# Kernel optimization log

Hardware: AMD Instinct MI355X
Metric: run time of the kernel (lower is better)

Reference implementation:

```python
import jax, jax.numpy as jnp
import numpy as np

H = 256
EPS = 1e-5
RBF_GAMMA = 10.0
RBF_CENTERS = jnp.asarray(np.arange(0.0, np.pi, 0.1), dtype=jnp.float32)  # 32 centers


def layer_norm(x, g, b):
    m = x.mean(-1, keepdims=True)
    v = ((x - m) ** 2).mean(-1, keepdims=True)
    return (x - m) * jax.lax.rsqrt(v + EPS) * g + b


def gin(src, dst, n_nodes, node_feat, edge_feat, w1, b1, w2, b2):
    # message = h_src + h_edge ; sum-aggregate at dst ; 2-layer MLP
    msg = node_feat[src] + edge_feat                                  # [E, H]
    agg = jax.ops.segment_sum(msg, dst, num_segments=n_nodes)        # [N, H]
    return jax.nn.relu(agg @ w1 + b1) @ w2 + b2


def graph_normal(gid, n_graphs, x):
    # divide each node feature by sqrt(#nodes in its graph)
    cnt = jax.ops.segment_sum(jnp.ones((x.shape[0],), x.dtype), gid, num_segments=n_graphs)
    return x * jax.lax.rsqrt(jnp.maximum(cnt, 1.0))[gid][:, None]


def geognn_block(src, dst, gid, n_graphs, node_hidden, edge_feat, w1, b1, w2, b2, ln_g, ln_b):
    out = gin(src, dst, node_hidden.shape[0], node_hidden, edge_feat, w1, b1, w2, b2)
    out = layer_norm(out, ln_g, ln_b)
    out = graph_normal(gid, n_graphs, out)
    # activation=False, dropout is identity in eval mode
    return out + node_hidden


def setup_inputs() -> dict:
    key = jax.random.key(0)
    ks = jax.random.split(key, 24)
    N, E, A, G = 65536, 131072, 262144, 2048
    nC = RBF_CENTERS.shape[0]
    s = 1.0 / np.sqrt(H)
    inp = {
        "node_hidden": jax.random.normal(ks[0], (N, H), jnp.float32),
        "edge_hidden": jax.random.normal(ks[1], (E, H), jnp.float32),
        "bond_angle": jax.random.uniform(ks[2], (A,), jnp.float32) * np.float32(np.pi),
        "ab_src": jax.random.randint(ks[3], (N * 2,), 0, N).astype(jnp.int64)[:E],
        "ab_dst": jax.random.randint(ks[4], (E,), 0, N).astype(jnp.int64),
        "ba_src": jax.random.randint(ks[5], (A,), 0, E).astype(jnp.int64),
        "ba_dst": jax.random.randint(ks[6], (A,), 0, E).astype(jnp.int64),
        "node_gid": jnp.sort(jax.random.randint(ks[7], (N,), 0, G)).astype(jnp.int64),
        "bond_gid": jnp.sort(jax.random.randint(ks[8], (E,), 0, G)).astype(jnp.int64),
        "num_graphs": G,
        # bond-angle RBF linear
        "rbf_w": jax.random.normal(ks[9], (nC, H), jnp.float32) / np.sqrt(nC),
        "rbf_b": jnp.zeros((H,), jnp.float32),
        # bond_angle_gnn (GIN MLP + LayerNorm)
        "ba_w1": jax.random.normal(ks[10], (H, 2 * H), jnp.float32) * s,
        "ba_b1": jnp.zeros((2 * H,), jnp.float32),
        "ba_w2": jax.random.normal(ks[11], (2 * H, H), jnp.float32) * s,
        "ba_b2": jnp.zeros((H,), jnp.float32),
        "ba_ln_g": jnp.ones((H,), jnp.float32),
        "ba_ln_b": jnp.zeros((H,), jnp.float32),
        # atom_bond_gnn
        "ab_w1": jax.random.normal(ks[12], (H, 2 * H), jnp.float32) * s,
        "ab_b1": jnp.zeros((2 * H,), jnp.float32),
        "ab_w2": jax.random.normal(ks[13], (2 * H, H), jnp.float32) * s,
        "ab_b2": jnp.zeros((H,), jnp.float32),
        "ab_ln_g": jnp.ones((H,), jnp.float32),
        "ab_ln_b": jnp.zeros((H,), jnp.float32),
    }
    return inp


def reference(node_hidden, edge_hidden, bond_angle, ab_src, ab_dst, ba_src, ba_dst,
              node_gid, bond_gid, num_graphs, rbf_w, rbf_b,
              ba_w1, ba_b1, ba_w2, ba_b2, ba_ln_g, ba_ln_b,
              ab_w1, ab_b1, ab_w2, ab_b2, ab_ln_g, ab_ln_b):
    # RBF encode bond angles -> angle edge features [A, H]
    rbf = jnp.exp(-RBF_GAMMA * (bond_angle[:, None] - RBF_CENTERS[None, :]) ** 2)
    angle_hidden = rbf @ rbf_w + rbf_b
    # bond-angle GNN updates bond features (nodes of bond_angle graph)
    edge_out = geognn_block(ba_src, ba_dst, bond_gid, num_graphs,
                            edge_hidden, angle_hidden,
                            ba_w1, ba_b1, ba_w2, ba_b2, ba_ln_g, ba_ln_b)
    # atom-bond GNN updates atom features using updated bond features as edge feats
    node_out = geognn_block(ab_src, ab_dst, node_gid, num_graphs,
                            node_hidden, edge_out,
                            ab_w1, ab_b1, ab_w2, ab_b2, ab_ln_g, ab_ln_b)
    # average pooling over atoms per graph
    cnt = jax.ops.segment_sum(jnp.ones((node_out.shape[0],), node_out.dtype), node_gid,
                              num_segments=num_graphs)
    graph_repr = jax.ops.segment_sum(node_out, node_gid, num_segments=num_graphs) / jnp.maximum(cnt, 1.0)[:, None]
    return node_out, edge_out, graph_repr
```

## Files before the change

kernel.cpp:

```cpp
#include <hip/hip_runtime.h>

#define HDIM 256
#define LNEPS 1e-5f

typedef float f32x4 __attribute__((ext_vector_type(4)));
typedef short bf16x8 __attribute__((ext_vector_type(8)));

static __device__ __forceinline__ unsigned short f2b(float f) {
  union { float f; unsigned u; } v; v.f = f;
  return (unsigned short)((v.u + 0x7fffu + ((v.u >> 16) & 1u)) >> 16);
}
static __device__ __forceinline__ unsigned pk2(float lo, float hi) {
  return (unsigned)f2b(lo) | ((unsigned)f2b(hi) << 16);
}

__global__ void pack_all_kernel(const float* __restrict__ w1a, const float* __restrict__ w2a,
                                const float* __restrict__ w1b, const float* __restrict__ w2b,
                                unsigned short* __restrict__ o1a, unsigned short* __restrict__ o2a,
                                unsigned short* __restrict__ o1b, unsigned short* __restrict__ o2b) {
  int sel = blockIdx.x >> 9;
  int o = (blockIdx.x & 511) * 256 + threadIdx.x;
  int ke = o & 7, lane = (o >> 3) & 63, tt = (o >> 9) & 1, w = (o >> 10) & 3, sl = o >> 12;
  int l15 = lane & 15, lg = lane >> 4;
  if (sel == 0 || sel == 2) {
    const float* in = (sel == 0) ? w1a : w1b;
    unsigned short* out = (sel == 0) ? o1a : o1b;
    int h = sl >> 3, kk = sl & 7;
    int n1 = h * 128 + w * 32 + tt * 16 + l15;
    int k = kk * 32 + lg * 8 + ke;
    out[o] = f2b(in[k * 512 + n1]);
  } else {
    const float* in = (sel == 1) ? w2a : w2b;
    unsigned short* out = (sel == 1) ? o2a : o2b;
    int h = sl >> 3, q = sl & 7, h2 = q >> 2, kk2 = q & 3;
    int n2 = h2 * 128 + w * 32 + tt * 16 + l15;
    int k2 = h * 128 + kk2 * 32 + lg * 8 + ke;
    out[o] = f2b(in[k2 * 256 + n2]);
  }
}

__global__ void prep_kernel(const int* __restrict__ node_gid, const int* __restrict__ bond_gid,
                            const int* __restrict__ ab_dst, const int* __restrict__ ba_dst,
                            int* cnt_node, int* cnt_bond, int* deg_n, int* deg_e,
                            int N, int E, int A) {
  int i = blockIdx.x * 256 + threadIdx.x;
  if (i < N) atomicAdd(&cnt_node[node_gid[i]], 1);
  if (i < E) {
    atomicAdd(&cnt_bond[bond_gid[i]], 1);
    atomicAdd(&deg_n[ab_dst[i]], 1);
  }
  if (i < A) atomicAdd(&deg_e[ba_dst[i]], 1);
}

__global__ void scan1_both_kernel(const int* __restrict__ degE, const int* __restrict__ degN,
                                  int* __restrict__ offE, int* __restrict__ offN,
                                  int* __restrict__ bsum, int E, int N, int nbE) {
  int b = blockIdx.x;
  const int* deg; int* excl; int* bs; int n; int bb;
  if (b < nbE) { deg = degE; excl = offE; bs = bsum; n = E; bb = b; }
  else { deg = degN; excl = offN; bs = bsum + 512; n = N; bb = b - nbE; }
  int t = threadIdx.x;
  int i = bb * 256 + t;
  int v = (i < n) ? deg[i] : 0;
  int lane = t & 63, w = t >> 6;
  int s = v;
#pragma unroll
  for (int d = 1; d < 64; d <<= 1) {
    int u = __shfl_up(s, d);
    if (lane >= d) s += u;
  }
  __shared__ int wsum[4];
  if (lane == 63) wsum[w] = s;
  __syncthreads();
  int base = 0;
  for (int ww = 0; ww < w; ++ww) base += wsum[ww];
  if (i < n) excl[i] = base + s - v;
  if (t == 255) bs[bb] = base + s;
}

__global__ void scan2_both_kernel(int* __restrict__ bsum, int nbE, int nbN) {
  int* bs = bsum + blockIdx.x * 512;
  int nb = (blockIdx.x == 0) ? nbE : nbN;
  int t = threadIdx.x;
  int v = (t < nb) ? bs[t] : 0;
  int lane = t & 63, w = t >> 6;
  int s = v;
#pragma unroll
  for (int d = 1; d < 64; d <<= 1) {
    int u = __shfl_up(s, d);
    if (lane >= d) s += u;
  }
  __shared__ int wsum[16];
  if (lane == 63) wsum[w] = s;
  __syncthreads();
  int base = 0;
  for (int ww = 0; ww < w; ++ww) base += wsum[ww];
  if (t < nb) bs[t] = base + s - v;
}

__global__ void scan3f_kernel(int* __restrict__ offE, int* __restrict__ offN,
                              const int* __restrict__ bsum,
                              const int* __restrict__ cnt_node, const int* __restrict__ cnt_bond,
                              float* fac_node, float* fac_bond, float* recip_node,
                              int E, int N, int G, int nbE, int nbN) {
  int b = blockIdx.x;
  if (b < nbE) {
    int i = b * 256 + threadIdx.x;
    if (i < E) offE[i] += bsum[b];
  } else if (b < nbE + nbN) {
    int bb = b - nbE;
    int i = bb * 256 + threadIdx.x;
    if (i < N) offN[i] += bsum[512 + bb];
  } else {
    int g = (b - nbE - nbN) * 256 + threadIdx.x;
    if (g < G) {
      float cn = fmaxf((float)cnt_node[g], 1.f);
      float cb = fmaxf((float)cnt_bond[g], 1.f);
      fac_node[g] = rsqrtf(cn);
      fac_bond[g] = rsqrtf(cb);
      recip_node[g] = 1.f / cn;
    }
  }
}

__global__ void fill_both_kernel(const int* __restrict__ ba_dst, const int* __restrict__ ab_dst,
                                 const int* __restrict__ offE, const int* __restrict__ offN,
                                 int* __restrict__ curE, int* __restrict__ curN,
                                 int* __restrict__ csrE, int* __restrict__ csrN,
                                 int A, int E, int nbA) {
  int b = blockIdx.x;
  if (b < nbA) {
    int i = b * 256 + threadIdx.x;
    if (i < A) {
      int d = ba_dst[i];
      int p = atomicAdd(&curE[d], 1);
      csrE[offE[d] + p] = i;
    }
  } else {
    int i = (b - nbA) * 256 + threadIdx.x;
    if (i < E) {
      int d = ab_dst[i];
      int p = atomicAdd(&curN[d], 1);
      csrN[offN[d] + p] = i;
    }
  }
}

__global__ __launch_bounds__(256) void angle_gather_kernel(
    const float* __restrict__ bond_angle, const int* __restrict__ ba_src,
    const float* __restrict__ edge_hidden,
    const int* __restrict__ off, const int* __restrict__ deg, const int* __restrict__ csr,
    const float* __restrict__ rbf_w, const float* __restrict__ rbf_b,
    float* __restrict__ agg_e, int E) {
  __shared__ float rbfw_s[32 * 256];
  int t = threadIdx.x;
  int w = t >> 6, lane = t & 63;
#pragma unroll
  for (int i = 0; i < 8; ++i)
    *(f32x4*)&rbfw_s[(t + i * 256) * 4] = *(const f32x4*)&rbf_w[(t + i * 256) * 4];
  __syncthreads();
  int c4 = lane * 4;
  f32x4 bv = *(const f32x4*)&rbf_b[c4];
  float cc = 0.1f * (float)(lane & 31);
  for (int rr = 0; rr < 4; ++rr) {
    int d = blockIdx.x * 16 + w * 4 + rr;
    if (d >= E) break;
    int start = off[d], cnt = deg[d];
    f32x4 acc = (f32x4)0.f;
    float rbfs = 0.f;
    for (int base = 0; base < cnt; base += 64) {
      int n = cnt - base; if (n > 64) n = 64;
      float av = 0.f;
      int s = 0;
      if (lane < n) {
        int a = csr[start + base + lane];
        av = bond_angle[a];
        s = ba_src[a];
      }
#pragma unroll 4
      for (int i = 0; i < n; ++i) {
        float avi = __shfl(av, i);
        int si = __shfl(s, i);
        if (lane < 32) {
          float dd = avi - cc;
          rbfs += __expf(-10.f * dd * dd);
        }
        acc += *(const f32x4*)&edge_hidden[(size_t)si * HDIM + c4];
      }
    }
#pragma unroll 8
    for (int k = 0; k < 32; ++k) {
      float rv = __shfl(rbfs, k);
      f32x4 wv = *(const f32x4*)&rbfw_s[k * 256 + c4];
      acc[0] += rv * wv[0]; acc[1] += rv * wv[1];
      acc[2] += rv * wv[2]; acc[3] += rv * wv[3];
    }
    float fc = (float)cnt;
    acc[0] += fc * bv[0]; acc[1] += fc * bv[1];
    acc[2] += fc * bv[2]; acc[3] += fc * bv[3];
    *(f32x4*)&agg_e[(size_t)d * HDIM + c4] = acc;
  }
}

__global__ __launch_bounds__(256) void node_gather_kernel(
    const float* __restrict__ node_hidden, const float* __restrict__ edge_out,
    const int* __restrict__ ab_src,
    const int* __restrict__ off, const int* __restrict__ deg, const int* __restrict__ csr,
    float* __restrict__ agg_n, int N) {
  int w = threadIdx.x >> 6, lane = threadIdx.x & 63;
  int d = blockIdx.x * 4 + w;
  if (d >= N) return;
  int c4 = lane * 4;
  int start = off[d], cnt = deg[d];
  f32x4 acc = (f32x4)0.f;
  for (int base = 0; base < cnt; base += 64) {
    int n = cnt - base; if (n > 64) n = 64;
    int e = 0, s = 0;
    if (lane < n) {
      e = csr[start + base + lane];
      s = ab_src[e];
    }
#pragma unroll 4
    for (int i = 0; i < n; ++i) {
      int ei = __shfl(e, i);
      int si = __shfl(s, i);
      f32x4 a = *(const f32x4*)&edge_out[(size_t)ei * HDIM + c4];
      f32x4 b = *(const f32x4*)&node_hidden[(size_t)si * HDIM + c4];
      acc += a;
      acc += b;
    }
  }
  *(f32x4*)&agg_n[(size_t)d * HDIM + c4] = acc;
}

template <int POOL>
__global__ __launch_bounds__(256, 4) void mlp_kernel(
    const float* agg_in, float* out_rows,
    const float* __restrict__ residual, const int* __restrict__ gid,
    const float* __restrict__ gfactor, const float* __restrict__ grecip,
    const unsigned short* __restrict__ w1p, const float* __restrict__ b1,
    const unsigned short* __restrict__ w2p, const float* __restrict__ b2,
    const float* __restrict__ ln_g, const float* __restrict__ ln_b,
    float* pool_out, int M) {
  __shared__ __align__(16) char smem[34432];
  char* Xb = smem;
  char* Hb = smem + 16384;
  char* OutsB = smem;
  float* psA = (float*)(smem + 32768);
  float* psB = (float*)(smem + 33280);
  float* fstat = (float*)(smem + 33792);
  float* gfs = (float*)(smem + 34048);
  float* grs = (float*)(smem + 34176);
  int* gid_s = (int*)(smem + 34304);

  int t = threadIdx.x;
  int row0 = blockIdx.x * 32;
  int w = t >> 6, lane = t & 63;
  int l15 = lane & 15, lg = lane >> 4;

  const unsigned short* w1f = w1p + ((size_t)(w * 2) * 64 + lane) * 8;
  const unsigned short* w2f = w2p + ((size_t)(w * 2) * 64 + lane) * 8;
#define W1F(hh, kk, tt) (*(const bf16x8*)(w1f + (size_t)((hh) * 8 + (kk)) * 4096 + (tt) * 512))
#define W2F(hh, q, nf) (*(const bf16x8*)(w2f + (size_t)((hh) * 8 + (q)) * 4096 + (nf) * 512))

  bf16x8 wcur0, wcur1, wnxt0, wnxt1;
  wcur0 = W1F(0, 0, 0);
  wcur1 = W1F(0, 0, 1);

  {
    int row = t >> 3;
    int c0 = (t & 7) * 32;
    int gr = row0 + row; if (gr >= M) gr = M - 1;
    const float* src = agg_in + (size_t)gr * HDIM + c0;
#pragma unroll
    for (int i = 0; i < 4; ++i) {
      f32x4 a = *(const f32x4*)(src + i * 8);
      f32x4 b = *(const f32x4*)(src + i * 8 + 4);
      int byte = (row * 512 + (c0 + i * 8) * 2) ^ ((row & 7) << 4);
      *(uint4*)(Xb + byte) =
          make_uint4(pk2(a[0], a[1]), pk2(a[2], a[3]), pk2(b[0], b[1]), pk2(b[2], b[3]));
    }
  }
  __syncthreads();

  f32x4 acc2[2][4];
#pragma unroll
  for (int mt = 0; mt < 2; ++mt)
#pragma unroll
    for (int nf = 0; nf < 4; ++nf) acc2[mt][nf] = (f32x4)0.f;

  for (int h = 0; h < 4; ++h) {
    f32x4 acc1[2][2];
#pragma unroll
    for (int tt = 0; tt < 2; ++tt)
#pragma unroll
      for (int mt = 0; mt < 2; ++mt) acc1[tt][mt] = (f32x4)0.f;

#pragma unroll
    for (int kk = 0; kk < 8; ++kk) {
      if (kk < 7) {
        wnxt0 = W1F(h, kk + 1, 0);
        wnxt1 = W1F(h, kk + 1, 1);
      } else {
        wnxt0 = W2F(h, 0, 0);
        wnxt1 = W2F(h, 0, 1);
      }
      bf16x8 xfr0, xfr1;
      {
        int byte0 = (l15 * 512 + kk * 64 + lg * 16) ^ ((l15 & 7) << 4);
        xfr0 = *(const bf16x8*)(Xb + byte0);
        int m = 16 + l15;
        int byte1 = (m * 512 + kk * 64 + lg * 16) ^ ((m & 7) << 4);
        xfr1 = *(const bf16x8*)(Xb + byte1);
      }
      acc1[0][0] = __builtin_amdgcn_mfma_f32_16x16x32_bf16(wcur0, xfr0, acc1[0][0], 0, 0, 0);
      acc1[0][1] = __builtin_amdgcn_mfma_f32_16x16x32_bf16(wcur0, xfr1, acc1[0][1], 0, 0, 0);
      acc1[1][0] = __builtin_amdgcn_mfma_f32_16x16x32_bf16(wcur1, xfr0, acc1[1][0], 0, 0, 0);
      acc1[1][1] = __builtin_amdgcn_mfma_f32_16x16x32_bf16(wcur1, xfr1, acc1[1][1], 0, 0, 0);
      wcur0 = wnxt0;
      wcur1 = wnxt1;
    }

#pragma unroll
    for (int tt = 0; tt < 2; ++tt) {
      f32x4 b1v = *(const f32x4*)&b1[h * 128 + w * 32 + tt * 16 + lg * 4];
#pragma unroll
      for (int mt = 0; mt < 2; ++mt) {
        f32x4 v = acc1[tt][mt] + b1v;
        v[0] = fmaxf(v[0], 0.f); v[1] = fmaxf(v[1], 0.f);
        v[2] = fmaxf(v[2], 0.f); v[3] = fmaxf(v[3], 0.f);
        int m = mt * 16 + l15;
        int n1l = w * 32 + tt * 16 + lg * 4;
        int byte = (m * 256 + n1l * 2) ^ ((m & 7) << 4);
        *(uint2*)(Hb + byte) = make_uint2(pk2(v[0], v[1]), pk2(v[2], v[3]));
      }
    }
    __syncthreads();

#pragma unroll
    for (int q = 0; q < 8; ++q) {
      if (q < 7) {
        wnxt0 = W2F(h, q + 1, 0);
        wnxt1 = W2F(h, q + 1, 1);
      } else if (h < 3) {
        wnxt0 = W1F(h + 1, 0, 0);
        wnxt1 = W1F(h + 1, 0, 1);
      }
      int kk2 = q & 3, h2 = q >> 2;
      bf16x8 hfr0, hfr1;
      {
        int byte0 = (l15 * 256 + kk2 * 64 + lg * 16) ^ ((l15 & 7) << 4);
        hfr0 = *(const bf16x8*)(Hb + byte0);
        int m = 16 + l15;
        int byte1 = (m * 256 + kk2 * 64 + lg * 16) ^ ((m & 7) << 4);
        hfr1 = *(const bf16x8*)(Hb + byte1);
      }
      acc2[0][h2 * 2 + 0] = __builtin_amdgcn_mfma_f32_16x16x32_bf16(hfr0, wcur0, acc2[0][h2 * 2 + 0], 0, 0, 0);
      acc2[0][h2 * 2 + 1] = __builtin_amdgcn_mfma_f32_16x16x32_bf16(hfr0, wcur1, acc2[0][h2 * 2 + 1], 0, 0, 0);
      acc2[1][h2 * 2 + 0] = __builtin_amdgcn_mfma_f32_16x16x32_bf16(hfr1, wcur0, acc2[1][h2 * 2 + 0], 0, 0, 0);
      acc2[1][h2 * 2 + 1] = __builtin_amdgcn_mfma_f32_16x16x32_bf16(hfr1, wcur1, acc2[1][h2 * 2 + 1], 0, 0, 0);
      wcur0 = wnxt0;
      wcur1 = wnxt1;
    }
    __syncthreads();
  }
#undef W1F
#undef W2F

  {
    float rs[2][4], rss[2][4];
#pragma unroll
    for (int mt = 0; mt < 2; ++mt)
#pragma unroll
      for (int jr = 0; jr < 4; ++jr) { rs[mt][jr] = 0.f; rss[mt][jr] = 0.f; }
#pragma unroll
    for (int nfi = 0; nfi < 4; ++nfi) {
      int col = (nfi >> 1) * 128 + w * 32 + (nfi & 1) * 16 + l15;
      float b2v = b2[col];
#pragma unroll
      for (int mt = 0; mt < 2; ++mt)
#pragma unroll
        for (int jr = 0; jr < 4; ++jr) {
          float v = acc2[mt][nfi][jr] + b2v;
          int row = mt * 16 + lg * 4 + jr;
          *(float*)(OutsB + (((row * 256 + col) * 4) ^ ((row & 7) << 4))) = v;
          rs[mt][jr] += v;
          rss[mt][jr] += v * v;
        }
    }
#pragma unroll
    for (int mt = 0; mt < 2; ++mt)
#pragma unroll
      for (int jr = 0; jr < 4; ++jr) {
        float sv = rs[mt][jr], ssv = rss[mt][jr];
        sv += __shfl_xor(sv, 1); ssv += __shfl_xor(ssv, 1);
        sv += __shfl_xor(sv, 2); ssv += __shfl_xor(ssv, 2);
        sv += __shfl_xor(sv, 4); ssv += __shfl_xor(ssv, 4);
        sv += __shfl_xor(sv, 8); ssv += __shfl_xor(ssv, 8);
        if (l15 == 0) {
          int r = mt * 16 + lg * 4 + jr;
          psA[r * 4 + w] = sv;
          psB[r * 4 + w] = ssv;
        }
      }
    if (t < 32) {
      int r = row0 + t;
      int g = (r < M) ? gid[r] : 0;
      gid_s[t] = g;
      gfs[t] = gfactor[g];
      if (POOL) grs[t] = grecip[g];
    }
  }
  __syncthreads();
  if (t < 32) {
    float sv = psA[t * 4] + psA[t * 4 + 1] + psA[t * 4 + 2] + psA[t * 4 + 3];
    float ssv = psB[t * 4] + psB[t * 4 + 1] + psB[t * 4 + 2] + psB[t * 4 + 3];
    float mean = sv * (1.f / 256.f);
    float var = ssv * (1.f / 256.f) - mean * mean;
    fstat[t * 2] = mean;
    fstat[t * 2 + 1] = rsqrtf(var + LNEPS);
  }
  __syncthreads();

  {
    float g_t = ln_g[t], bb_t = ln_b[t];
    float psum = 0.f;
    float currecip = 0.f;
    int curg = -1;
#pragma unroll 4
    for (int p = 0; p < 32; ++p) {
      int gr = row0 + p;
      if (gr < M) {
        float v = *(const float*)(OutsB + (((p * 256 + t) * 4) ^ ((p & 7) << 4)));
        v = (v - fstat[p * 2]) * fstat[p * 2 + 1] * g_t + bb_t;
        v *= gfs[p];
        v += residual[(size_t)gr * HDIM + t];
        out_rows[(size_t)gr * HDIM + t] = v;
        if (POOL) {
          int g = gid_s[p];
          if (g != curg) {
            if (curg >= 0) atomicAdd(&pool_out[(size_t)curg * HDIM + t], psum * currecip);
            psum = 0.f;
            curg = g;
            currecip = grs[p];
          }
          psum += v;
        }
      }
    }
    if (POOL && curg >= 0) atomicAdd(&pool_out[(size_t)curg * HDIM + t], psum * currecip);
  }
}

extern "C" void kernel_launch(void* const* d_in, const int* in_sizes, int n_in,
                              void* d_out, int out_size, void* d_ws, size_t ws_size,
                              hipStream_t stream) {
  const float* node_hidden = (const float*)d_in[0];
  const float* edge_hidden = (const float*)d_in[1];
  const float* bond_angle = (const float*)d_in[2];
  const int* ab_src = (const int*)d_in[3];
  const int* ab_dst = (const int*)d_in[4];
  const int* ba_src = (const int*)d_in[5];
  const int* ba_dst = (const int*)d_in[6];
  const int* node_gid = (const int*)d_in[7];
  const int* bond_gid = (const int*)d_in[8];
  const float* rbf_w = (const float*)d_in[10];
  const float* rbf_b = (const float*)d_in[11];
  const float* ba_w1 = (const float*)d_in[12];
  const float* ba_b1 = (const float*)d_in[13];
  const float* ba_w2 = (const float*)d_in[14];
  const float* ba_b2 = (const float*)d_in[15];
  const float* ba_ln_g = (const float*)d_in[16];
  const float* ba_ln_b = (const float*)d_in[17];
  const float* ab_w1 = (const float*)d_in[18];
  const float* ab_b1 = (const float*)d_in[19];
  const float* ab_w2 = (const float*)d_in[20];
  const float* ab_b2 = (const float*)d_in[21];
  const float* ab_ln_g = (const float*)d_in[22];
  const float* ab_ln_b = (const float*)d_in[23];

  int N = in_sizes[0] / HDIM;
  int E = in_sizes[1] / HDIM;
  int A = in_sizes[2];
  int G = out_size / HDIM - N - E;

  float* out_node = (float*)d_out;
  float* out_edge = out_node + (size_t)N * HDIM;
  float* out_graph = out_edge + (size_t)E * HDIM;

  char* ws = (char*)d_ws;
  int* cnt_node = (int*)ws;
  int* cnt_bond = cnt_node + G;
  int* deg_e = cnt_bond + G;
  int* cur_e = deg_e + E;
  int* deg_n = cur_e + E;
  int* cur_n = deg_n + N;
  size_t zero_bytes = (size_t)(2 * G + 2 * E + 2 * N) * 4;
  float* fac_node = (float*)(cur_n + N);
  float* fac_bond = fac_node + G;
  float* recip_node = fac_bond + G;
  int* off_e = (int*)(recip_node + G);
  int* csr_e = off_e + E;
  int* off_n = csr_e + A;
  int* csr_n = off_n + N;
  int* bsum = csr_n + E;
  size_t off = ((size_t)((char*)(bsum + 1024) - ws) + 255) & ~(size_t)255;
  unsigned short* w1p_ba = (unsigned short*)(ws + off); off += (size_t)512 * 256 * 2;
  unsigned short* w2p_ba = (unsigned short*)(ws + off); off += (size_t)256 * 512 * 2;
  unsigned short* w1p_ab = (unsigned short*)(ws + off); off += (size_t)512 * 256 * 2;
  unsigned short* w2p_ab = (unsigned short*)(ws + off); off += (size_t)256 * 512 * 2;

  hipMemsetAsync(d_ws, 0, zero_bytes, stream);
  hipMemsetAsync(out_graph, 0, (size_t)G * HDIM * 4, stream);

  pack_all_kernel<<<2048, 256, 0, stream>>>(ba_w1, ba_w2, ab_w1, ab_w2,
                                            w1p_ba, w2p_ba, w1p_ab, w2p_ab);

  prep_kernel<<<(A + 255) / 256, 256, 0, stream>>>(node_gid, bond_gid, ab_dst, ba_dst,
                                                   cnt_node, cnt_bond, deg_n, deg_e, N, E, A);

  int nbE = (E + 255) / 256;
  int nbN = (N + 255) / 256;
  int nbA = (A + 255) / 256;
  int nbG = (G + 255) / 256;
  scan1_both_kernel<<<nbE + nbN, 256, 0, stream>>>(deg_e, deg_n, off_e, off_n, bsum, E, N, nbE);
  scan2_both_kernel<<<2, 1024, 0, stream>>>(bsum, nbE, nbN);
  scan3f_kernel<<<nbE + nbN + nbG, 256, 0, stream>>>(off_e, off_n, bsum, cnt_node, cnt_bond,
                                                     fac_node, fac_bond, recip_node,
                                                     E, N, G, nbE, nbN);
  fill_both_kernel<<<nbA + nbE, 256, 0, stream>>>(ba_dst, ab_dst, off_e, off_n,
                                                  cur_e, cur_n, csr_e, csr_n, A, E, nbA);

  angle_gather_kernel<<<(E + 15) / 16, 256, 0, stream>>>(bond_angle, ba_src, edge_hidden,
                                                         off_e, deg_e, csr_e, rbf_w, rbf_b,
                                                         out_edge, E);
  mlp_kernel<0><<<(E + 31) / 32, 256, 0, stream>>>(out_edge, out_edge, edge_hidden, bond_gid,
                                                   fac_bond, nullptr, w1p_ba, ba_b1, w2p_ba,
                                                   ba_b2, ba_ln_g, ba_ln_b, nullptr, E);

  node_gather_kernel<<<(N + 3) / 4, 256, 0, stream>>>(node_hidden, out_edge, ab_src,
                                                      off_n, deg_n, csr_n, out_node, N);
  mlp_kernel<1><<<(N + 31) / 32, 256, 0, stream>>>(out_node, out_node, node_hidden, node_gid,
                                                   fac_node, recip_node, w1p_ab, ab_b1, w2p_ab,
                                                   ab_b2, ab_ln_g, ab_ln_b, out_graph, N);
}
```

Before: 567.7 us.

## Tile MLP kernel to 64 rows with 8 waves and register-resident LayerNorm epilogue

The fused GIN MLP kernel now processes 64 rows per block with 512 threads, arranged as 2 row groups by 4 column groups. This lets the two row groups share weight fragments through cache and doubles the rows covered per block. The LayerNorm, graph-normal, residual and pooling epilogue now works directly from the MFMA accumulators instead of staging the output tile through LDS and re-reading it. The graph-id loads are hoisted to the start of the kernel. In exchange, global stores become narrower per-lane scalar writes, pooling issues more atomics, and the tighter launch bounds with larger LDS use may lower occupancy or cause register spills.

```diff
diff --git a/kernel.cpp b/kernel.cpp
--- a/kernel.cpp
+++ b/kernel.cpp
@@ -234,7 +234,7 @@
 }
 
 template <int POOL>
-__global__ __launch_bounds__(256, 4) void mlp_kernel(
+__global__ __launch_bounds__(512, 6) void mlp_kernel(
     const float* agg_in, float* out_rows,
     const float* __restrict__ residual, const int* __restrict__ gid,
     const float* __restrict__ gfactor, const float* __restrict__ grecip,
@@ -242,24 +242,24 @@
     const unsigned short* __restrict__ w2p, const float* __restrict__ b2,
     const float* __restrict__ ln_g, const float* __restrict__ ln_b,
     float* pool_out, int M) {
-  __shared__ __align__(16) char smem[34432];
+  __shared__ __align__(16) char smem[52480];
   char* Xb = smem;
-  char* Hb = smem + 16384;
-  char* OutsB = smem;
-  float* psA = (float*)(smem + 32768);
-  float* psB = (float*)(smem + 33280);
-  float* fstat = (float*)(smem + 33792);
-  float* gfs = (float*)(smem + 34048);
-  float* grs = (float*)(smem + 34176);
-  int* gid_s = (int*)(smem + 34304);
+  char* Hb = smem + 32768;
+  float* psA = (float*)(smem + 49152);
+  float* psB = (float*)(smem + 50176);
+  float* fstat = (float*)(smem + 51200);
+  float* gfs = (float*)(smem + 51712);
+  float* grs = (float*)(smem + 51968);
+  int* gid_s = (int*)(smem + 52224);
 
   int t = threadIdx.x;
-  int row0 = blockIdx.x * 32;
-  int w = t >> 6, lane = t & 63;
+  int row0 = blockIdx.x * 64;
+  int w8 = t >> 6, lane = t & 63;
+  int wr = w8 >> 2, wc = w8 & 3;
   int l15 = lane & 15, lg = lane >> 4;
 
-  const unsigned short* w1f = w1p + ((size_t)(w * 2) * 64 + lane) * 8;
-  const unsigned short* w2f = w2p + ((size_t)(w * 2) * 64 + lane) * 8;
+  const unsigned short* w1f = w1p + ((size_t)(wc * 2) * 64 + lane) * 8;
+  const unsigned short* w2f = w2p + ((size_t)(wc * 2) * 64 + lane) * 8;
 #define W1F(hh, kk, tt) (*(const bf16x8*)(w1f + (size_t)((hh) * 8 + (kk)) * 4096 + (tt) * 512))
 #define W2F(hh, q, nf) (*(const bf16x8*)(w2f + (size_t)((hh) * 8 + (q)) * 4096 + (nf) * 512))
 
@@ -279,6 +279,13 @@
       int byte = (row * 512 + (c0 + i * 8) * 2) ^ ((row & 7) << 4);
       *(uint4*)(Xb + byte) =
           make_uint4(pk2(a[0], a[1]), pk2(a[2], a[3]), pk2(b[0], b[1]), pk2(b[2], b[3]));
+    }
+    if (t < 64) {
+      int r = row0 + t;
+      int g = (r < M) ? gid[r] : 0;
+      gid_s[t] = g;
+      gfs[t] = gfactor[g];
+      if (POOL) grs[t] = grecip[g];
     }
   }
   __syncthreads();
@@ -307,10 +314,11 @@
       }
       bf16x8 xfr0, xfr1;
       {
-        int byte0 = (l15 * 512 + kk * 64 + lg * 16) ^ ((l15 & 7) << 4);
+        int m0 = wr * 32 + l15;
+        int byte0 = (m0 * 512 + kk * 64 + lg * 16) ^ ((m0 & 7) << 4);
         xfr0 = *(const bf16x8*)(Xb + byte0);
-        int m = 16 + l15;
-        int byte1 = (m * 512 + kk * 64 + lg * 16) ^ ((m & 7) << 4);
+        int m1 = wr * 32 + 16 + l15;
+        int byte1 = (m1 * 512 + kk * 64 + lg * 16) ^ ((m1 & 7) << 4);
         xfr1 = *(const bf16x8*)(Xb + byte1);
       }
       acc1[0][0] = __builtin_amdgcn_mfma_f32_16x16x32_bf16(wcur0, xfr0, acc1[0][0], 0, 0, 0);
@@ -323,14 +331,14 @@
 
 #pragma unroll
     for (int tt = 0; tt < 2; ++tt) {
-      f32x4 b1v = *(const f32x4*)&b1[h * 128 + w * 32 + tt * 16 + lg * 4];
+      f32x4 b1v = *(const f32x4*)&b1[h * 128 + wc * 32 + tt * 16 + lg * 4];
 #pragma unroll
       for (int mt = 0; mt < 2; ++mt) {
         f32x4 v = acc1[tt][mt] + b1v;
         v[0] = fmaxf(v[0], 0.f); v[1] = fmaxf(v[1], 0.f);
         v[2] = fmaxf(v[2], 0.f); v[3] = fmaxf(v[3], 0.f);
-        int m = mt * 16 + l15;
-        int n1l = w * 32 + tt * 16 + lg * 4;
+        int m = wr * 32 + mt * 16 + l15;
+        int n1l = wc * 32 + tt * 16 + lg * 4;
         int byte = (m * 256 + n1l * 2) ^ ((m & 7) << 4);
         *(uint2*)(Hb + byte) = make_uint2(pk2(v[0], v[1]), pk2(v[2], v[3]));
       }
@@ -349,10 +357,11 @@
       int kk2 = q & 3, h2 = q >> 2;
       bf16x8 hfr0, hfr1;
       {
-        int byte0 = (l15 * 256 + kk2 * 64 + lg * 16) ^ ((l15 & 7) << 4);
+        int m0 = wr * 32 + l15;
+        int byte0 = (m0 * 256 + kk2 * 64 + lg * 16) ^ ((m0 & 7) << 4);
         hfr0 = *(const bf16x8*)(Hb + byte0);
-        int m = 16 + l15;
-        int byte1 = (m * 256 + kk2 * 64 + lg * 16) ^ ((m & 7) << 4);
+        int m1 = wr * 32 + 16 + l15;
+        int byte1 = (m1 * 256 + kk2 * 64 + lg * 16) ^ ((m1 & 7) << 4);
         hfr1 = *(const bf16x8*)(Hb + byte1);
       }
       acc2[0][h2 * 2 + 0] = __builtin_amdgcn_mfma_f32_16x16x32_bf16(hfr0, wcur0, acc2[0][h2 * 2 + 0], 0, 0, 0);
@@ -368,51 +377,31 @@
 #undef W2F
 
   {
-    float rs[2][4], rss[2][4];
 #pragma unroll
     for (int mt = 0; mt < 2; ++mt)
 #pragma unroll
-      for (int jr = 0; jr < 4; ++jr) { rs[mt][jr] = 0.f; rss[mt][jr] = 0.f; }
-#pragma unroll
-    for (int nfi = 0; nfi < 4; ++nfi) {
-      int col = (nfi >> 1) * 128 + w * 32 + (nfi & 1) * 16 + l15;
-      float b2v = b2[col];
-#pragma unroll
-      for (int mt = 0; mt < 2; ++mt)
-#pragma unroll
-        for (int jr = 0; jr < 4; ++jr) {
-          float v = acc2[mt][nfi][jr] + b2v;
-          int row = mt * 16 + lg * 4 + jr;
-          *(float*)(OutsB + (((row * 256 + col) * 4) ^ ((row & 7) << 4))) = v;
-          rs[mt][jr] += v;
-          rss[mt][jr] += v * v;
+      for (int jr = 0; jr < 4; ++jr) {
+        float sv = 0.f, ssv = 0.f;
+#pragma unroll
+        for (int nfi = 0; nfi < 4; ++nfi) {
+          int col = (nfi >> 1) * 128 + wc * 32 + (nfi & 1) * 16 + l15;
+          float v = acc2[mt][nfi][jr] + b2[col];
+          sv += v;
+          ssv += v * v;
         }
-    }
-#pragma unroll
-    for (int mt = 0; mt < 2; ++mt)
-#pragma unroll
-      for (int jr = 0; jr < 4; ++jr) {
-        float sv = rs[mt][jr], ssv = rss[mt][jr];
         sv += __shfl_xor(sv, 1); ssv += __shfl_xor(ssv, 1);
         sv += __shfl_xor(sv, 2); ssv += __shfl_xor(ssv, 2);
         sv += __shfl_xor(sv, 4); ssv += __shfl_xor(ssv, 4);
         sv += __shfl_xor(sv, 8); ssv += __shfl_xor(ssv, 8);
         if (l15 == 0) {
-          int r = mt * 16 + lg * 4 + jr;
-          psA[r * 4 + w] = sv;
-          psB[r * 4 + w] = ssv;
+          int r = wr * 32 + mt * 16 + lg * 4 + jr;
+          psA[r * 4 + wc] = sv;
+          psB[r * 4 + wc] = ssv;
         }
       }
-    if (t < 32) {
-      int r = row0 + t;
-      int g = (r < M) ? gid[r] : 0;
-      gid_s[t] = g;
-      gfs[t] = gfactor[g];
-      if (POOL) grs[t] = grecip[g];
-    }
   }
   __syncthreads();
-  if (t < 32) {
+  if (t < 64) {
     float sv = psA[t * 4] + psA[t * 4 + 1] + psA[t * 4 + 2] + psA[t * 4 + 3];
     float ssv = psB[t * 4] + psB[t * 4 + 1] + psB[t * 4 + 2] + psB[t * 4 + 3];
     float mean = sv * (1.f / 256.f);
@@ -423,32 +412,52 @@
   __syncthreads();
 
   {
-    float g_t = ln_g[t], bb_t = ln_b[t];
-    float psum = 0.f;
-    float currecip = 0.f;
+    int c0 = wc * 32 + l15, c1 = c0 + 16, c2 = c0 + 128, c3 = c0 + 144;
+    float b2v0 = b2[c0], b2v1 = b2[c1], b2v2 = b2[c2], b2v3 = b2[c3];
+    float lgm0 = ln_g[c0], lgm1 = ln_g[c1], lgm2 = ln_g[c2], lgm3 = ln_g[c3];
+    float lbm0 = ln_b[c0], lbm1 = ln_b[c1], lbm2 = ln_b[c2], lbm3 = ln_b[c3];
+    float p0 = 0.f, p1 = 0.f, p2 = 0.f, p3 = 0.f;
+    float crec = 0.f;
     int curg = -1;
-#pragma unroll 4
-    for (int p = 0; p < 32; ++p) {
-      int gr = row0 + p;
-      if (gr < M) {
-        float v = *(const float*)(OutsB + (((p * 256 + t) * 4) ^ ((p & 7) << 4)));
-        v = (v - fstat[p * 2]) * fstat[p * 2 + 1] * g_t + bb_t;
-        v *= gfs[p];
-        v += residual[(size_t)gr * HDIM + t];
-        out_rows[(size_t)gr * HDIM + t] = v;
-        if (POOL) {
-          int g = gid_s[p];
-          if (g != curg) {
-            if (curg >= 0) atomicAdd(&pool_out[(size_t)curg * HDIM + t], psum * currecip);
-            psum = 0.f;
-            curg = g;
-            currecip = grs[p];
+#pragma unroll
+    for (int mt = 0; mt < 2; ++mt) {
+#pragma unroll
+      for (int jr = 0; jr < 4; ++jr) {
+        int r = wr * 32 + mt * 16 + lg * 4 + jr;
+        int gr = row0 + r;
+        if (gr < M) {
+          float mean = fstat[r * 2], rstd = fstat[r * 2 + 1];
+          float gf = gfs[r];
+          if (POOL) {
+            int g = gid_s[r];
+            if (g != curg) {
+              if (curg >= 0) {
+                atomicAdd(&pool_out[(size_t)curg * HDIM + c0], p0 * crec);
+                atomicAdd(&pool_out[(size_t)curg * HDIM + c1], p1 * crec);
+                atomicAdd(&pool_out[(size_t)curg * HDIM + c2], p2 * crec);
+                atomicAdd(&pool_out[(size_t)curg * HDIM + c3], p3 * crec);
+              }
+              curg = g; crec = grs[r];
+              p0 = 0.f; p1 = 0.f; p2 = 0.f; p3 = 0.f;
+            }
           }
-          psum += v;
+          const float* resp = residual + (size_t)gr * HDIM;
+          float* outp = out_rows + (size_t)gr * HDIM;
+          float v0 = ((acc2[mt][0][jr] + b2v0 - mean) * rstd * lgm0 + lbm0) * gf + resp[c0];
+          float v1 = ((acc2[mt][1][jr] + b2v1 - mean) * rstd * lgm1 + lbm1) * gf + resp[c1];
+          float v2 = ((acc2[mt][2][jr] + b2v2 - mean) * rstd * lgm2 + lbm2) * gf + resp[c2];
+          float v3 = ((acc2[mt][3][jr] + b2v3 - mean) * rstd * lgm3 + lbm3) * gf + resp[c3];
+          outp[c0] = v0; outp[c1] = v1; outp[c2] = v2; outp[c3] = v3;
+          if (POOL) { p0 += v0; p1 += v1; p2 += v2; p3 += v3; }
         }
       }
     }
-    if (POOL && curg >= 0) atomicAdd(&pool_out[(size_t)curg * HDIM + t], psum * currecip);
+    if (POOL && curg >= 0) {
+      atomicAdd(&pool_out[(size_t)curg * HDIM + c0], p0 * crec);
+      atomicAdd(&pool_out[(size_t)curg * HDIM + c1], p1 * crec);
+      atomicAdd(&pool_out[(size_t)curg * HDIM + c2], p2 * crec);
+      atomicAdd(&pool_out[(size_t)curg * HDIM + c3], p3 * crec);
+    }
   }
 }
 
@@ -534,13 +543,13 @@
   angle_gather_kernel<<<(E + 15) / 16, 256, 0, stream>>>(bond_angle, ba_src, edge_hidden,
                                                          off_e, deg_e, csr_e, rbf_w, rbf_b,
                                                          out_edge, E);
-  mlp_kernel<0><<<(E + 31) / 32, 256, 0, stream>>>(out_edge, out_edge, edge_hidden, bond_gid,
+  mlp_kernel<0><<<(E + 63) / 64, 512, 0, stream>>>(out_edge, out_edge, edge_hidden, bond_gid,
                                                    fac_bond, nullptr, w1p_ba, ba_b1, w2p_ba,
                                                    ba_b2, ba_ln_g, ba_ln_b, nullptr, E);
 
   node_gather_kernel<<<(N + 3) / 4, 256, 0, stream>>>(node_hidden, out_edge, ab_src,
                                                       off_n, deg_n, csr_n, out_node, N);
-  mlp_kernel<1><<<(N + 31) / 32, 256, 0, stream>>>(out_node, out_node, node_hidden, node_gid,
+  mlp_kernel<1><<<(N + 63) / 64, 512, 0, stream>>>(out_node, out_node, node_hidden, node_gid,
                                                    fac_node, recip_node, w1p_ab, ab_b1, w2p_ab,
                                                    ab_b2, ab_ln_g, ab_ln_b, out_graph, N);
 }
```

Result: slower. 678.9 us (+19.6%).
